# Kernel tuning notes

Hardware: AMD Instinct MI355X
Metric: run time of the kernel (lower is better)

The kernel has to match this reference:

```python
import jax, jax.numpy as jnp
import numpy as np

B, S, H, E = 2, 2048, 16, 64
INV_SCALE = 8.0  # sqrt(head_dim); forward divides scores by this


def setup_inputs() -> dict:
    key = jax.random.key(0)
    ks = jax.random.split(key, 10)
    return {
        "query": jax.random.normal(ks[0], (B, S, H, E), dtype=jnp.float32),
        "key": jax.random.normal(ks[1], (B, S, H, E), dtype=jnp.float32),
        "value": jax.random.normal(ks[2], (B, S, H, E), dtype=jnp.float32),
        "attn_mask": jax.random.randint(ks[3], (B, S), 0, 2, dtype=jnp.int32),
        "Wq": jax.random.normal(ks[4], (E, E), dtype=jnp.float32) / np.sqrt(E),
        "bq": jax.random.normal(ks[5], (E,), dtype=jnp.float32) * 0.02,
        "Wk": jax.random.normal(ks[6], (E, E), dtype=jnp.float32) / np.sqrt(E),
        "bk": jax.random.normal(ks[7], (E,), dtype=jnp.float32) * 0.02,
        "Wv": jax.random.normal(ks[8], (E, E), dtype=jnp.float32) / np.sqrt(E),
        "bv": jax.random.normal(ks[9], (E,), dtype=jnp.float32) * 0.02,
    }


def reference(query, key, value, attn_mask, Wq, bq, Wk, bk, Wv, bv):
    # Linear projections over the last (embed) dim; torch Linear: x @ W.T + b
    q = jnp.einsum('bshe,fe->bhsf', query, Wq) + bq  # [B,H,S,E] (permute 0,2,1,3 fused)
    k = jnp.einsum('bshe,fe->bhsf', key, Wk) + bk
    v = jnp.einsum('bshe,fe->bhsf', value, Wv) + bv
    scores = jnp.einsum('bhqe,bhke->bhqk', q, k) / INV_SCALE  # [B,H,S,S]
    # mask: positions where attn_mask == 0 get -inf, broadcast over (1,1,k_len)
    masked = attn_mask[:, None, None, :] == 0  # [B,1,1,S]
    scores = jnp.where(masked, -jnp.inf, scores)
    attn = jax.nn.softmax(scores, axis=-1)
    out = jnp.einsum('bhqk,bhke->bqhe', attn, v)  # permute back to [B,S,H,E]
    return out
```

## Files before the change

### kernel.cpp

```cpp
#include <hip/hip_runtime.h>


#define BATCH 2
#define SEQ   2048
#define NH    16
#define DE    64
#define LDP   72
#define LDOF  68
#define NKT   (SEQ / 64)
#define LOG2E 1.44269504088896340736f

using bf16x8   = __attribute__((ext_vector_type(8))) __bf16;
using bf16x4   = __attribute__((ext_vector_type(4))) __bf16;
using floatx4  = __attribute__((ext_vector_type(4))) float;
using floatx16 = __attribute__((ext_vector_type(16))) float;
using ushortx4 = __attribute__((ext_vector_type(4))) unsigned short;
using ushortx8 = __attribute__((ext_vector_type(8))) unsigned short;

__device__ __forceinline__ ushortx4 cvt4(floatx4 f) {
    bf16x4 h = __builtin_convertvector(f, bf16x4);
    return __builtin_bit_cast(ushortx4, h);
}

__device__ __forceinline__ void glds16(const unsigned short* g, unsigned short* l) {
    __builtin_amdgcn_global_load_lds(
        (const __attribute__((address_space(1))) unsigned int*)g,
        (__attribute__((address_space(3))) unsigned int*)l, 16, 0, 0);
}

__global__ __launch_bounds__(256) void proj_kernel(
    const float* __restrict__ xq, const float* __restrict__ xk, const float* __restrict__ xv,
    const float* __restrict__ Wq, const float* __restrict__ bq,
    const float* __restrict__ Wk, const float* __restrict__ bk,
    const float* __restrict__ Wv, const float* __restrict__ bv,
    unsigned short* __restrict__ qb, unsigned short* __restrict__ kb,
    unsigned short* __restrict__ vtb)
{
    __shared__ __align__(16) unsigned short Xb[64 * LDP];
    __shared__ __align__(16) unsigned short Wb[64 * LDP];
    __shared__ __align__(16) unsigned short Ob[64 * LDP];
    __shared__ float blds[64];

    const int t  = threadIdx.x;
    const int p  = blockIdx.x >> 10;
    const int bh = (blockIdx.x >> 5) & 31;
    const int st = blockIdx.x & 31;
    const int s0 = st * 64;
    const int b  = bh >> 4, h = bh & 15;
    const int lane = t & 63, w = t >> 6, quad = lane >> 4, l16 = lane & 15;

    const float* x    = (p == 0) ? xq : (p == 1) ? xk : xv;
    const float* W    = (p == 0) ? Wq : (p == 1) ? Wk : Wv;
    const float* bias = (p == 0) ? bq : (p == 1) ? bk : bv;

    #pragma unroll
    for (int i = 0; i < 4; ++i) {
        int idx = i * 1024 + t * 4;
        int row = idx >> 6, col = idx & 63;
        floatx4 xv4 = *(const floatx4*)(x + (((size_t)(b * SEQ + s0 + row) * NH + h) * DE + col));
        *(ushortx4*)&Xb[row * LDP + col] = cvt4(xv4);
        floatx4 wv4 = *(const floatx4*)(W + row * 64 + col);
        *(ushortx4*)&Wb[row * LDP + col] = cvt4(wv4);
    }
    if (t < 64) blds[t] = bias[t];
    __syncthreads();

    if (p < 2) {
        bf16x8 a0 = *(const bf16x8*)&Wb[(w * 16 + l16) * LDP + quad * 8];
        bf16x8 a1 = *(const bf16x8*)&Wb[(w * 16 + l16) * LDP + 32 + quad * 8];
        floatx4 bf4 = *(const floatx4*)&blds[w * 16 + quad * 4];
        const float scale = (p == 0) ? 0.125f * LOG2E : 1.0f;
        #pragma unroll
        for (int nb = 0; nb < 4; ++nb) {
            bf16x8 b0 = *(const bf16x8*)&Xb[(nb * 16 + l16) * LDP + quad * 8];
            bf16x8 b1 = *(const bf16x8*)&Xb[(nb * 16 + l16) * LDP + 32 + quad * 8];
            floatx4 c = {0.f, 0.f, 0.f, 0.f};
            c = __builtin_amdgcn_mfma_f32_16x16x32_bf16(a0, b0, c, 0, 0, 0);
            c = __builtin_amdgcn_mfma_f32_16x16x32_bf16(a1, b1, c, 0, 0, 0);
            floatx4 v;
            v[0] = (c[0] + bf4[0]) * scale; v[1] = (c[1] + bf4[1]) * scale;
            v[2] = (c[2] + bf4[2]) * scale; v[3] = (c[3] + bf4[3]) * scale;
            *(ushortx4*)&Ob[(nb * 16 + l16) * LDP + w * 16 + quad * 4] = cvt4(v);
        }
    } else {
        bf16x8 a0 = *(const bf16x8*)&Xb[(w * 16 + l16) * LDP + quad * 8];
        bf16x8 a1 = *(const bf16x8*)&Xb[(w * 16 + l16) * LDP + 32 + quad * 8];
        #pragma unroll
        for (int nb = 0; nb < 4; ++nb) {
            bf16x8 b0 = *(const bf16x8*)&Wb[(nb * 16 + l16) * LDP + quad * 8];
            bf16x8 b1 = *(const bf16x8*)&Wb[(nb * 16 + l16) * LDP + 32 + quad * 8];
            floatx4 c = {0.f, 0.f, 0.f, 0.f};
            c = __builtin_amdgcn_mfma_f32_16x16x32_bf16(a0, b0, c, 0, 0, 0);
            c = __builtin_amdgcn_mfma_f32_16x16x32_bf16(a1, b1, c, 0, 0, 0);
            float bw = blds[nb * 16 + l16];
            floatx4 v;
            v[0] = c[0] + bw; v[1] = c[1] + bw; v[2] = c[2] + bw; v[3] = c[3] + bw;
            *(ushortx4*)&Ob[(nb * 16 + l16) * LDP + w * 16 + quad * 4] = cvt4(v);
        }
    }
    __syncthreads();

    #pragma unroll
    for (int j = 0; j < 2; ++j) {
        int idx = j * 256 + t;
        int row = idx >> 3, c = idx & 7;
        int cp  = (c ^ (row & 7)) * 8;
        ushortx8 v = *(const ushortx8*)&Ob[row * LDP + c * 8];
        if (p < 2) {
            unsigned short* dst = (p == 0) ? qb : kb;
            *(ushortx8*)(dst + ((size_t)bh * SEQ + s0 + row) * DE + cp) = v;
        } else {
            *(ushortx8*)(vtb + ((size_t)bh * DE + row) * SEQ + s0 + cp) = v;
        }
    }
}

__global__ __launch_bounds__(256) void attn_kernel(
    const unsigned short* __restrict__ qb, const unsigned short* __restrict__ kb,
    const unsigned short* __restrict__ vtb, const int* __restrict__ mask,
    float* __restrict__ out)
{
    __shared__ __align__(16) char smem[16384 * 3 + 512];
    unsigned short* Kl = (unsigned short*)smem;
    unsigned short* Vl = (unsigned short*)(smem + 16384);
    unsigned short* Pq = (unsigned short*)(smem + 32768);
    float*          Ml = (float*)(smem + 49152);
    float*          Ol = (float*)smem;

    const int t  = threadIdx.x;
    const int qt = blockIdx.x, bh = blockIdx.y;
    const int b  = bh >> 4, h = bh & 15;
    const int q0 = qt * 128;
    const int lane = t & 63, w = t >> 6;
    const int l31 = lane & 31, hl = lane >> 5;
    const int sw  = l31 & 7;
    const int qrow = w * 32 + l31;

    const unsigned short* kbase = kb + (size_t)bh * SEQ * DE;
    const unsigned short* vbase = vtb + (size_t)bh * DE * SEQ;
    const unsigned short* qsrc  = qb + ((size_t)bh * SEQ + q0) * DE;
    const int* mrow = mask + b * SEQ;

    #pragma unroll
    for (int u = 0; u < 4; ++u)
        glds16(qsrc + (w * 32 + u * 8 + (lane >> 3)) * DE + (lane & 7) * 8,
               Pq + (w * 32 + u * 8) * 64);
    glds16(kbase + (size_t)(w * 16 + (lane >> 3)) * DE + (lane & 7) * 8,     Kl + w * 1024);
    glds16(kbase + (size_t)(w * 16 + 8 + (lane >> 3)) * DE + (lane & 7) * 8, Kl + w * 1024 + 512);
    glds16(vbase + (size_t)(w * 16 + (lane >> 3)) * SEQ + (lane & 7) * 8,     Vl + w * 1024);
    glds16(vbase + (size_t)(w * 16 + 8 + (lane >> 3)) * SEQ + (lane & 7) * 8, Vl + w * 1024 + 512);
    if (t < 64) Ml[t] = mrow[t] ? -16.0f : -1e30f;
    int mreg = (t < 64) ? mrow[64 + t] : 0;
    __syncthreads();

    bf16x8 qf[4];
    #pragma unroll
    for (int estep = 0; estep < 4; ++estep)
        qf[estep] = *(const bf16x8*)&Pq[qrow * 64 + ((2 * estep + hl) ^ sw) * 8];

    float l_i = 0.f;
    floatx16 oacc[2];
    #pragma unroll
    for (int eh = 0; eh < 2; ++eh)
        #pragma unroll
        for (int r = 0; r < 16; ++r) oacc[eh][r] = 0.f;

    for (int kt = 0; kt < NKT; ++kt) {
        const int cur = kt & 1, nxt = cur ^ 1;
        const unsigned short* Kc = Kl + cur * 4096;
        const unsigned short* Vc = Vl + cur * 4096;
        const float*          Mc = Ml + cur * 64;

        if (kt + 1 < NKT) {
            const int k1 = (kt + 1) * 64;
            glds16(kbase + (size_t)(k1 + w * 16 + (lane >> 3)) * DE + (lane & 7) * 8,
                   Kl + nxt * 4096 + w * 1024);
            glds16(kbase + (size_t)(k1 + w * 16 + 8 + (lane >> 3)) * DE + (lane & 7) * 8,
                   Kl + nxt * 4096 + w * 1024 + 512);
            glds16(vbase + (size_t)(w * 16 + (lane >> 3)) * SEQ + k1 + (lane & 7) * 8,
                   Vl + nxt * 4096 + w * 1024);
            glds16(vbase + (size_t)(w * 16 + 8 + (lane >> 3)) * SEQ + k1 + (lane & 7) * 8,
                   Vl + nxt * 4096 + w * 1024 + 512);
            if (t < 64) Ml[nxt * 64 + t] = mreg ? -16.0f : -1e30f;
            mreg = (t < 64 && kt + 2 < NKT) ? mrow[(kt + 2) * 64 + t] : 0;
        }

        float sum = 0.f;
        #pragma unroll
        for (int kh = 0; kh < 2; ++kh) {
            floatx16 c;
            #pragma unroll
            for (int g = 0; g < 4; ++g) {
                floatx4 mg = *(const floatx4*)&Mc[kh * 32 + g * 8 + hl * 4];
                c[g * 4 + 0] = mg[0]; c[g * 4 + 1] = mg[1];
                c[g * 4 + 2] = mg[2]; c[g * 4 + 3] = mg[3];
            }
            #pragma unroll
            for (int estep = 0; estep < 4; ++estep) {
                bf16x8 kf = *(const bf16x8*)&Kc[(kh * 32 + l31) * 64 + ((2 * estep + hl) ^ sw) * 8];
                c = __builtin_amdgcn_mfma_f32_32x32x16_bf16(kf, qf[estep], c, 0, 0, 0);
            }
            #pragma unroll
            for (int r = 0; r < 16; ++r) {
                c[r] = __builtin_amdgcn_exp2f(c[r]);
                sum += c[r];
            }
            #pragma unroll
            for (int m = 0; m < 4; ++m) {
                floatx4 g4 = {c[4 * m + 0], c[4 * m + 1], c[4 * m + 2], c[4 * m + 3]};
                *(ushortx4*)&Pq[qrow * 64 + (((m + 4 * kh) ^ sw) * 8) + hl * 4] = cvt4(g4);
            }
        }
        sum += __shfl_xor(sum, 32);
        l_i += sum;
        __asm__ volatile("s_waitcnt lgkmcnt(0)" ::: "memory");

        bf16x8 pf[4];
        #pragma unroll
        for (int kstep = 0; kstep < 4; ++kstep)
            pf[kstep] = *(const bf16x8*)&Pq[qrow * 64 + ((2 * kstep + hl) ^ sw) * 8];

        #pragma unroll
        for (int eh = 0; eh < 2; ++eh)
            #pragma unroll
            for (int kstep = 0; kstep < 4; ++kstep) {
                bf16x8 vf = *(const bf16x8*)&Vc[(eh * 32 + l31) * 64 + ((2 * kstep + hl) ^ sw) * 8];
                oacc[eh] = __builtin_amdgcn_mfma_f32_32x32x16_bf16(vf, pf[kstep], oacc[eh], 0, 0, 0);
            }

        __syncthreads();
    }

    __syncthreads();
    float invl = __builtin_amdgcn_rcpf(l_i);
    #pragma unroll
    for (int eh = 0; eh < 2; ++eh)
        #pragma unroll
        for (int m = 0; m < 4; ++m) {
            floatx4 ov;
            ov[0] = oacc[eh][4 * m + 0] * invl; ov[1] = oacc[eh][4 * m + 1] * invl;
            ov[2] = oacc[eh][4 * m + 2] * invl; ov[3] = oacc[eh][4 * m + 3] * invl;
            *(floatx4*)&Ol[qrow * LDOF + eh * 32 + m * 8 + hl * 4] = ov;
        }
    __syncthreads();
    #pragma unroll
    for (int pass = 0; pass < 8; ++pass) {
        int rl  = pass * 16 + (t >> 4);
        int col = (t & 15) * 4;
        floatx4 tv = *(const floatx4*)&Ol[rl * LDOF + col];
        *(floatx4*)(out + (((size_t)b * SEQ + q0 + rl) * NH + h) * DE + col) = tv;
    }
}

extern "C" void kernel_launch(void* const* d_in, const int* in_sizes, int n_in,
                              void* d_out, int out_size, void* d_ws, size_t ws_size,
                              hipStream_t stream) {
    const float* query = (const float*)d_in[0];
    const float* key   = (const float*)d_in[1];
    const float* value = (const float*)d_in[2];
    const int*   mask  = (const int*)d_in[3];
    const float* Wq = (const float*)d_in[4];
    const float* bq = (const float*)d_in[5];
    const float* Wk = (const float*)d_in[6];
    const float* bk = (const float*)d_in[7];
    const float* Wv = (const float*)d_in[8];
    const float* bv = (const float*)d_in[9];

    const size_t tensor_elems = (size_t)BATCH * NH * SEQ * DE;
    unsigned short* qb  = (unsigned short*)d_ws;
    unsigned short* kb  = qb + tensor_elems;
    unsigned short* vtb = kb + tensor_elems;

    proj_kernel<<<dim3(3 * BATCH * NH * (SEQ / 64)), 256, 0, stream>>>(
        query, key, value, Wq, bq, Wk, bk, Wv, bv, qb, kb, vtb);
    attn_kernel<<<dim3(SEQ / 128, BATCH * NH), 256, 0, stream>>>(
        qb, kb, vtb, mask, (float*)d_out);
}
```

Baseline: 163.6 us.

## Double attention query tile to 256 rows with 512-thread blocks

The attention kernel now handles 256 query rows per block with 8 waves instead of 128 rows with 4 waves. Each K/V tile staged in LDS is shared by twice as many query rows, halving global and LDS load traffic per query. Each thread now issues one K and one V async load per tile instead of two. The P staging buffer switches from an XOR-swizzled layout to a padded row stride, and a barrier is added after the Q fragments are read so P writes cannot overwrite them. The cost is fewer blocks (256) and a larger LDS footprint that fully reuses the buffer for the output transpose, which may reduce latency hiding.

```diff
diff --git a/kernel.cpp b/kernel.cpp
--- a/kernel.cpp
+++ b/kernel.cpp
@@ -8,6 +8,7 @@
 #define LDP   72
 #define LDOF  68
 #define NKT   (SEQ / 64)
+#define QT    256
 #define LOG2E 1.44269504088896340736f
 
 using bf16x8   = __attribute__((ext_vector_type(8))) __bf16;
@@ -115,22 +116,22 @@
     }
 }
 
-__global__ __launch_bounds__(256) void attn_kernel(
+__global__ __launch_bounds__(512) void attn_kernel(
     const unsigned short* __restrict__ qb, const unsigned short* __restrict__ kb,
     const unsigned short* __restrict__ vtb, const int* __restrict__ mask,
     float* __restrict__ out)
 {
-    __shared__ __align__(16) char smem[16384 * 3 + 512];
+    __shared__ __align__(16) char smem[16384 + 16384 + 36864 + 512];
     unsigned short* Kl = (unsigned short*)smem;
     unsigned short* Vl = (unsigned short*)(smem + 16384);
     unsigned short* Pq = (unsigned short*)(smem + 32768);
-    float*          Ml = (float*)(smem + 49152);
+    float*          Ml = (float*)(smem + 32768 + 36864);
     float*          Ol = (float*)smem;
 
     const int t  = threadIdx.x;
     const int qt = blockIdx.x, bh = blockIdx.y;
     const int b  = bh >> 4, h = bh & 15;
-    const int q0 = qt * 128;
+    const int q0 = qt * QT;
     const int lane = t & 63, w = t >> 6;
     const int l31 = lane & 31, hl = lane >> 5;
     const int sw  = l31 & 7;
@@ -143,12 +144,9 @@
 
     #pragma unroll
     for (int u = 0; u < 4; ++u)
-        glds16(qsrc + (w * 32 + u * 8 + (lane >> 3)) * DE + (lane & 7) * 8,
-               Pq + (w * 32 + u * 8) * 64);
-    glds16(kbase + (size_t)(w * 16 + (lane >> 3)) * DE + (lane & 7) * 8,     Kl + w * 1024);
-    glds16(kbase + (size_t)(w * 16 + 8 + (lane >> 3)) * DE + (lane & 7) * 8, Kl + w * 1024 + 512);
-    glds16(vbase + (size_t)(w * 16 + (lane >> 3)) * SEQ + (lane & 7) * 8,     Vl + w * 1024);
-    glds16(vbase + (size_t)(w * 16 + 8 + (lane >> 3)) * SEQ + (lane & 7) * 8, Vl + w * 1024 + 512);
+        glds16(qsrc + (u * 8 + w) * 512 + lane * 8, Pq + (u * 8 + w) * 512);
+    glds16(kbase + (size_t)(w * 8 + (lane >> 3)) * DE + (lane & 7) * 8,  Kl + w * 512);
+    glds16(vbase + (size_t)(w * 8 + (lane >> 3)) * SEQ + (lane & 7) * 8, Vl + w * 512);
     if (t < 64) Ml[t] = mrow[t] ? -16.0f : -1e30f;
     int mreg = (t < 64) ? mrow[64 + t] : 0;
     __syncthreads();
@@ -156,7 +154,7 @@
     bf16x8 qf[4];
     #pragma unroll
     for (int estep = 0; estep < 4; ++estep)
-        qf[estep] = *(const bf16x8*)&Pq[qrow * 64 + ((2 * estep + hl) ^ sw) * 8];
+        qf[estep] = *(const bf16x8*)&Pq[qrow * 64 + (((2 * estep + hl) ^ sw) * 8)];
 
     float l_i = 0.f;
     floatx16 oacc[2];
@@ -164,6 +162,7 @@
     for (int eh = 0; eh < 2; ++eh)
         #pragma unroll
         for (int r = 0; r < 16; ++r) oacc[eh][r] = 0.f;
+    __syncthreads();
 
     for (int kt = 0; kt < NKT; ++kt) {
         const int cur = kt & 1, nxt = cur ^ 1;
@@ -173,14 +172,10 @@
 
         if (kt + 1 < NKT) {
             const int k1 = (kt + 1) * 64;
-            glds16(kbase + (size_t)(k1 + w * 16 + (lane >> 3)) * DE + (lane & 7) * 8,
-                   Kl + nxt * 4096 + w * 1024);
-            glds16(kbase + (size_t)(k1 + w * 16 + 8 + (lane >> 3)) * DE + (lane & 7) * 8,
-                   Kl + nxt * 4096 + w * 1024 + 512);
-            glds16(vbase + (size_t)(w * 16 + (lane >> 3)) * SEQ + k1 + (lane & 7) * 8,
-                   Vl + nxt * 4096 + w * 1024);
-            glds16(vbase + (size_t)(w * 16 + 8 + (lane >> 3)) * SEQ + k1 + (lane & 7) * 8,
-                   Vl + nxt * 4096 + w * 1024 + 512);
+            glds16(kbase + (size_t)(k1 + w * 8 + (lane >> 3)) * DE + (lane & 7) * 8,
+                   Kl + nxt * 4096 + w * 512);
+            glds16(vbase + (size_t)(w * 8 + (lane >> 3)) * SEQ + k1 + (lane & 7) * 8,
+                   Vl + nxt * 4096 + w * 512);
             if (t < 64) Ml[nxt * 64 + t] = mreg ? -16.0f : -1e30f;
             mreg = (t < 64 && kt + 2 < NKT) ? mrow[(kt + 2) * 64 + t] : 0;
         }
@@ -197,7 +192,7 @@
             }
             #pragma unroll
             for (int estep = 0; estep < 4; ++estep) {
-                bf16x8 kf = *(const bf16x8*)&Kc[(kh * 32 + l31) * 64 + ((2 * estep + hl) ^ sw) * 8];
+                bf16x8 kf = *(const bf16x8*)&Kc[(kh * 32 + l31) * 64 + (((2 * estep + hl) ^ sw) * 8)];
                 c = __builtin_amdgcn_mfma_f32_32x32x16_bf16(kf, qf[estep], c, 0, 0, 0);
             }
             #pragma unroll
@@ -208,7 +203,7 @@
             #pragma unroll
             for (int m = 0; m < 4; ++m) {
                 floatx4 g4 = {c[4 * m + 0], c[4 * m + 1], c[4 * m + 2], c[4 * m + 3]};
-                *(ushortx4*)&Pq[qrow * 64 + (((m + 4 * kh) ^ sw) * 8) + hl * 4] = cvt4(g4);
+                *(ushortx4*)&Pq[qrow * LDP + (4 * kh + m) * 8 + hl * 4] = cvt4(g4);
             }
         }
         sum += __shfl_xor(sum, 32);
@@ -218,20 +213,19 @@
         bf16x8 pf[4];
         #pragma unroll
         for (int kstep = 0; kstep < 4; ++kstep)
-            pf[kstep] = *(const bf16x8*)&Pq[qrow * 64 + ((2 * kstep + hl) ^ sw) * 8];
+            pf[kstep] = *(const bf16x8*)&Pq[qrow * LDP + (2 * kstep + hl) * 8];
 
         #pragma unroll
         for (int eh = 0; eh < 2; ++eh)
             #pragma unroll
             for (int kstep = 0; kstep < 4; ++kstep) {
-                bf16x8 vf = *(const bf16x8*)&Vc[(eh * 32 + l31) * 64 + ((2 * kstep + hl) ^ sw) * 8];
+                bf16x8 vf = *(const bf16x8*)&Vc[(eh * 32 + l31) * 64 + (((2 * kstep + hl) ^ sw) * 8)];
                 oacc[eh] = __builtin_amdgcn_mfma_f32_32x32x16_bf16(vf, pf[kstep], oacc[eh], 0, 0, 0);
             }
 
         __syncthreads();
     }
 
-    __syncthreads();
     float invl = __builtin_amdgcn_rcpf(l_i);
     #pragma unroll
     for (int eh = 0; eh < 2; ++eh)
@@ -245,8 +239,9 @@
     __syncthreads();
     #pragma unroll
     for (int pass = 0; pass < 8; ++pass) {
-        int rl  = pass * 16 + (t >> 4);
-        int col = (t & 15) * 4;
+        int idx = pass * 512 + t;
+        int rl  = idx >> 4;
+        int col = (idx & 15) * 4;
         floatx4 tv = *(const floatx4*)&Ol[rl * LDOF + col];
         *(floatx4*)(out + (((size_t)b * SEQ + q0 + rl) * NH + h) * DE + col) = tv;
     }
@@ -273,6 +268,6 @@
 
     proj_kernel<<<dim3(3 * BATCH * NH * (SEQ / 64)), 256, 0, stream>>>(
         query, key, value, Wq, bq, Wk, bk, Wv, bv, qb, kb, vtb);
-    attn_kernel<<<dim3(SEQ / 128, BATCH * NH), 256, 0, stream>>>(
+    attn_kernel<<<dim3(SEQ / QT, BATCH * NH), 512, 0, stream>>>(
         qb, kb, vtb, mask, (float*)d_out);
 }
```

After: 156.8 us. 4.2% less time.
